# Performance work log

Measured on AMD Instinct MI355X. Metric: run time of the kernel, lower is better.

The kernel has to match this reference:

```python
import jax, jax.numpy as jnp
import numpy as np

H = 8          # attention heads
L = 2          # gnn_layers
D = 256        # embedding_size (= per-head out channels)
NEG_SLOPE = 0.2
LN_EPS = 1e-5


def setup_inputs() -> dict:
    key = jax.random.key(0)
    ks = jax.random.split(key, 10)
    B, N, E = 8, 4096, 131072
    node_embeddings = jax.random.normal(ks[0], (B, N, D), dtype=jnp.float32)
    edges = jax.random.randint(ks[1], (B, 2, E), 0, N, dtype=jnp.int64)
    s = 1.0 / np.sqrt(D)
    W       = jax.random.normal(ks[2], (L, H * D, D), dtype=jnp.float32) * s   # GATConv lin weight
    att_src = jax.random.normal(ks[3], (L, H, D), dtype=jnp.float32) * s
    att_dst = jax.random.normal(ks[4], (L, H, D), dtype=jnp.float32) * s
    gat_bias = jnp.zeros((L, H * D), dtype=jnp.float32)
    lin_W   = jax.random.normal(ks[5], (L, D, H * D), dtype=jnp.float32) * (1.0 / np.sqrt(H * D))
    lin_b   = jnp.zeros((L, D), dtype=jnp.float32)
    ln_gamma = jnp.ones((D,), dtype=jnp.float32)
    ln_beta  = jnp.zeros((D,), dtype=jnp.float32)
    return {"node_embeddings": node_embeddings, "edges": edges, "W": W,
            "att_src": att_src, "att_dst": att_dst, "gat_bias": gat_bias,
            "lin_W": lin_W, "lin_b": lin_b, "ln_gamma": ln_gamma, "ln_beta": ln_beta}


def _gat_conv(x, edge_index, Wl, a_src, a_dst, bias):
    # x: [N, D]; edge_index: [2, E] (row0 = src j, row1 = dst i)
    N = x.shape[0]
    loops = jnp.arange(N, dtype=edge_index.dtype)
    src = jnp.concatenate([edge_index[0], loops])   # PyG add_self_loops=True
    dst = jnp.concatenate([edge_index[1], loops])
    h = (x @ Wl.T).reshape(N, H, D)                 # [N, H, D]
    a_s = jnp.sum(h * a_src, axis=-1)               # [N, H]
    a_d = jnp.sum(h * a_dst, axis=-1)               # [N, H]
    e = jax.nn.leaky_relu(a_s[src] + a_d[dst], NEG_SLOPE)   # [E+N, H]
    # softmax over incoming edges of each destination node
    emax = jax.ops.segment_max(e, dst, num_segments=N)
    ex = jnp.exp(e - emax[dst])
    denom = jax.ops.segment_sum(ex, dst, num_segments=N)
    alpha = ex / (denom[dst] + 1e-16)               # [E+N, H]
    msg = h[src] * alpha[:, :, None]                # [E+N, H, D]
    out = jax.ops.segment_sum(msg, dst, num_segments=N)     # [N, H, D]
    return out.reshape(N, H * D) + bias


def _layer_norm(x, gamma, beta):
    mu = jnp.mean(x, axis=-1, keepdims=True)
    var = jnp.mean(jnp.square(x - mu), axis=-1, keepdims=True)
    return (x - mu) * jax.lax.rsqrt(var + LN_EPS) * gamma + beta


def reference(node_embeddings, edges, W, att_src, att_dst, gat_bias, lin_W, lin_b, ln_gamma, ln_beta):
    def per_graph(x, ei):
        h = x
        for l in range(L):
            res = h
            g = _gat_conv(h, ei, W[l], att_src[l], att_dst[l], gat_bias[l])
            g = g @ lin_W[l].T + lin_b[l]
            g = _layer_norm(g, ln_gamma, ln_beta)
            h = jax.nn.relu(g + res)   # dropout is identity at inference
        return h
    return jax.vmap(per_graph)(node_embeddings, edges)
```

## Files before the change

### kernel.cpp

```cpp
#include <hip/hip_runtime.h>
#include <hip/hip_bf16.h>

#define BB 8
#define NN 4096
#define EE 131072
#define ENL (EE + NN)
#define DD 256
#define HH 8
#define HD 2048
#define NPB (BB * NN)
#define CHUNK 16384
#define CAP 128

typedef __attribute__((ext_vector_type(8))) short bf16x8;
typedef __attribute__((ext_vector_type(4))) float f32x4;

static __device__ __forceinline__ float bf_lo(unsigned int u) { return __uint_as_float(u << 16); }
static __device__ __forceinline__ float bf_hi(unsigned int u) { return __uint_as_float(u & 0xFFFF0000u); }
static __device__ __forceinline__ unsigned short f2bf(float f) {
    __hip_bfloat16 h = __float2bfloat16(f);
    return *reinterpret_cast<unsigned short*>(&h);
}
static __device__ __forceinline__ unsigned int pack2(float a, float b) {
    return ((unsigned)f2bf(b) << 16) | f2bf(a);
}
static __device__ __forceinline__ void load_lds16(const void* g, void* l) {
    __builtin_amdgcn_global_load_lds(
        (const __attribute__((address_space(1))) unsigned int*)(g),
        (__attribute__((address_space(3))) unsigned int*)(l), 16, 0, 0);
}
static __device__ __forceinline__ float rl_f(float v, int lane) {
    return __uint_as_float(__builtin_amdgcn_readlane(__float_as_uint(v), lane));
}

__global__ void k_scatter(const int* __restrict__ edges, int* __restrict__ cnt, int* __restrict__ col) {
    int b = blockIdx.y;
    int idx = blockIdx.x * 256 + threadIdx.x;
    if (idx >= ENL) return;
    int src, dst;
    if (idx < EE) { src = edges[b*2*EE + idx]; dst = edges[b*2*EE + EE + idx]; }
    else { src = dst = idx - EE; }
    int g = b * NN + dst;
    int pos = atomicAdd(&cnt[g], 1);
    if (pos < CAP) col[(size_t)g * CAP + pos] = src;
}

__global__ __launch_bounds__(256) void k_prepA(const float* __restrict__ W, const float* __restrict__ linW,
                                               unsigned short* __restrict__ M2t,
                                               const float* __restrict__ asrc, const float* __restrict__ adst,
                                               float* __restrict__ wsatt, float* __restrict__ wdatt) {
    __shared__ float red[2][4][64];
    int bx = blockIdx.x;
    if (bx < 512) {
        int cb = bx & 31, h = (bx >> 5) & 7, l = bx >> 8;
        int d = threadIdx.x;
        const float* Bp = W + ((size_t)l * HD + h * DD) * DD;
        const float* Ap = linW + ((size_t)l * DD + cb * 8) * HD + h * DD;
        float acc[8] = {};
        for (int o = 0; o < DD; ++o) {
            float w = Bp[(size_t)o * DD + d];
            #pragma unroll
            for (int c = 0; c < 8; ++c)
                acc[c] = fmaf(Ap[(size_t)c * HD + o], w, acc[c]);
        }
        #pragma unroll
        for (int c = 0; c < 8; ++c)
            M2t[((size_t)l * DD + cb * 8 + c) * HD + h * DD + d] = f2bf(acc[c]);
    } else {
        int idx = bx - 512;
        int kb = idx & 3, h = (idx >> 2) & 7, l = idx >> 5;
        int k = threadIdx.x & 63, dg = threadIdx.x >> 6;
        float accs = 0.f, accd = 0.f;
        #pragma unroll 4
        for (int dd = 0; dd < 64; ++dd) {
            int d = dg * 64 + dd;
            float w = W[((size_t)l * HD + h * DD + d) * DD + kb * 64 + k];
            accs = fmaf(asrc[(l*HH + h)*DD + d], w, accs);
            accd = fmaf(adst[(l*HH + h)*DD + d], w, accd);
        }
        red[0][dg][k] = accs; red[1][dg][k] = accd;
        __syncthreads();
        int t = threadIdx.x;
        if (t < 64)
            wsatt[(l*HH + h)*DD + kb*64 + t] = red[0][0][t] + red[0][1][t] + red[0][2][t] + red[0][3][t];
        else if (t < 128) {
            int kk = t - 64;
            wdatt[(l*HH + h)*DD + kb*64 + kk] = red[1][0][kk] + red[1][1][kk] + red[1][2][kk] + red[1][3][kk];
        }
    }
}

__global__ __launch_bounds__(256) void k_prepB(const float* __restrict__ gbias, const float* __restrict__ linW,
                                               const float* __restrict__ linb, float* __restrict__ bias2,
                                               const float* __restrict__ ws, const float* __restrict__ wd,
                                               unsigned short* __restrict__ frag) {
    int bx = blockIdx.x;
    if (bx < 128) {
        int wv = threadIdx.x >> 6, lane = threadIdx.x & 63;
        int o = bx * 4 + wv;
        int l = o >> 8, c = o & 255;
        const float4* g4 = (const float4*)(gbias + l * HD);
        const float4* w4 = (const float4*)(linW + (size_t)l * DD * HD + (size_t)c * HD);
        float acc = 0.f;
        #pragma unroll
        for (int j = 0; j < 8; ++j) {
            float4 g = g4[j * 64 + lane]; float4 w = w4[j * 64 + lane];
            acc += g.x * w.x + g.y * w.y + g.z * w.z + g.w * w.w;
        }
        #pragma unroll
        for (int msk = 1; msk < 64; msk <<= 1) acc += __shfl_xor(acc, msk);
        if (lane == 0) bias2[o] = acc + linb[o];
    } else {
        int idx = bx - 128;
        int l = idx >> 1;
        int t = (idx & 1) * 256 + threadIdx.x;
        int ks = t >> 6, lane = t & 63, c = lane & 15, q = lane >> 4;
        #pragma unroll
        for (int j = 0; j < 8; ++j) {
            int k = ks * 32 + q * 8 + j;
            float v = (c < 8) ? ws[(l*HH + c)*DD + k] : wd[(l*HH + (c-8))*DD + k];
            frag[((size_t)l * 512 + t) * 8 + j] = f2bf(v);
        }
    }
}

__global__ void k_tobf(const float* __restrict__ X, uint2* __restrict__ xb2) {
    int idx = blockIdx.x * 256 + threadIdx.x;
    float4 v = *(const float4*)(X + (size_t)idx * 4);
    uint2 o; o.x = pack2(v.x, v.y); o.y = pack2(v.z, v.w);
    xb2[idx] = o;
}

__global__ __launch_bounds__(256) void k_attn_mfma(const unsigned short* __restrict__ xb,
                                                   const unsigned short* __restrict__ attfrag,
                                                   float* __restrict__ a_s, float* __restrict__ a_d) {
    int tid = threadIdx.x;
    int wv = tid >> 6, lane = tid & 63;
    int m0 = blockIdx.x * 64 + wv * 16;
    int c = lane & 15, q = lane >> 4;
    const unsigned short* arow = xb + (size_t)(m0 + c) * DD;
    f32x4 acc = (f32x4){0.f, 0.f, 0.f, 0.f};
    #pragma unroll
    for (int ks = 0; ks < 8; ++ks) {
        bf16x8 af = *(const bf16x8*)(arow + ks * 32 + q * 8);
        bf16x8 bf = *(const bf16x8*)(attfrag + (size_t)(ks * 64 + lane) * 8);
        acc = __builtin_amdgcn_mfma_f32_16x16x32_bf16(af, bf, acc, 0, 0, 0);
    }
    #pragma unroll
    for (int rg = 0; rg < 4; ++rg) {
        int row = m0 + q * 4 + rg;
        if (c < 8) a_s[row * 8 + c] = acc[rg];
        else       a_d[row * 8 + (c - 8)] = acc[rg];
    }
}

__global__ __launch_bounds__(256) void k_agg_y(const int* __restrict__ cnt, const int* __restrict__ col,
                                               const float* __restrict__ a_s, const float* __restrict__ a_d,
                                               const uint2* __restrict__ xb2, uint2* __restrict__ y2,
                                               int node0) {
    int wave = threadIdx.x >> 6, lane = threadIdx.x & 63;
    int blk = blockIdx.x;
    int xcd = blk & 7, q = blk >> 3;
    int gl = xcd >> 1;
    int sub = ((xcd & 1) << 9) | q;
    int g = node0 + gl * NN + sub * 4 + wave;
    int b = g >> 12;
    int re = cnt[g];
    const int* cl = col + (size_t)g * CAP;
    int gb = b * NN;
    int hl = lane & 7, slot = lane >> 3;
    float adh = a_d[(size_t)g * 8 + hl];
    float acc[8][4] = {};
    float sacc = 0.f;
    int nfull = re & ~7;
    for (int e0 = 0; e0 < nfull; e0 += 8) {
        int srcl = cl[e0 + slot];
        float sg = a_s[(size_t)(gb + srcl) * 8 + hl];
        int ss[8];
        #pragma unroll
        for (int i = 0; i < 8; ++i) ss[i] = __builtin_amdgcn_readlane(srcl, i * 8);
        uint2 u[8];
        #pragma unroll
        for (int i = 0; i < 8; ++i)
            u[i] = xb2[(size_t)(gb + ss[i]) * 64 + lane];
        float xs = sg + adh;
        xs = (xs > 0.f) ? xs : 0.2f * xs;
        float w = __expf(xs);
        sacc += w;
        #pragma unroll
        for (int i = 0; i < 8; ++i) {
            float x0 = bf_lo(u[i].x), x1 = bf_hi(u[i].x), x2 = bf_lo(u[i].y), x3 = bf_hi(u[i].y);
            #pragma unroll
            for (int h = 0; h < 8; ++h) {
                float wh = rl_f(w, i * 8 + h);
                acc[h][0] = fmaf(wh, x0, acc[h][0]);
                acc[h][1] = fmaf(wh, x1, acc[h][1]);
                acc[h][2] = fmaf(wh, x2, acc[h][2]);
                acc[h][3] = fmaf(wh, x3, acc[h][3]);
            }
        }
    }
    if (nfull < re) {
        int e = nfull + slot;
        bool valid = e < re;
        int srcl = valid ? cl[e] : 0;
        float w = 0.f;
        if (valid) {
            float xs = a_s[(size_t)(gb + srcl) * 8 + hl] + adh;
            xs = (xs > 0.f) ? xs : 0.2f * xs;
            w = __expf(xs);
        }
        sacc += w;
        int cntl = re - nfull;
        for (int i = 0; i < cntl; ++i) {
            int s = __builtin_amdgcn_readlane(srcl, i * 8);
            uint2 u = xb2[(size_t)(gb + s) * 64 + lane];
            float x0 = bf_lo(u.x), x1 = bf_hi(u.x), x2 = bf_lo(u.y), x3 = bf_hi(u.y);
            #pragma unroll
            for (int h = 0; h < 8; ++h) {
                float wh = rl_f(w, i * 8 + h);
                acc[h][0] = fmaf(wh, x0, acc[h][0]);
                acc[h][1] = fmaf(wh, x1, acc[h][1]);
                acc[h][2] = fmaf(wh, x2, acc[h][2]);
                acc[h][3] = fmaf(wh, x3, acc[h][3]);
            }
        }
    }
    sacc += __shfl_xor(sacc, 8);
    sacc += __shfl_xor(sacc, 16);
    sacc += __shfl_xor(sacc, 32);
    float rinv = 1.f / (sacc + 1e-16f);
    uint2* yr = y2 + (size_t)(g - node0) * 512 + lane;
    #pragma unroll
    for (int h = 0; h < 8; ++h) {
        float rh = rl_f(rinv, h);
        uint2 o;
        o.x = pack2(acc[h][0] * rh, acc[h][1] * rh);
        o.y = pack2(acc[h][2] * rh, acc[h][3] * rh);
        yr[h * 64] = o;
    }
}

__global__ __launch_bounds__(512) void k_gemm_ln(const unsigned short* __restrict__ Yb,
                                                 const unsigned short* __restrict__ Bt,
                                                 const float* __restrict__ bias2,
                                                 const float* __restrict__ gamma,
                                                 const float* __restrict__ beta,
                                                 const float* __restrict__ res,
                                                 float* __restrict__ out,
                                                 unsigned int* __restrict__ xb,
                                                 int node0) {
    __shared__ char lds[86528];
    int tid = threadIdx.x;
    int wv = tid >> 6, lane = tid & 63;
    int m0 = blockIdx.x * 64;
    int c = lane & 15, q = lane >> 4;
    f32x4 acc[4][2];
    #pragma unroll
    for (int mf = 0; mf < 4; ++mf)
        #pragma unroll
        for (int nf = 0; nf < 2; ++nf) acc[mf][nf] = (f32x4){0.f, 0.f, 0.f, 0.f};

    #define STAGE(BUF, KT) do {                                                        \
        int row_ = tid >> 3, j_ = tid & 7, jp_ = j_ ^ (row_ & 7);                      \
        load_lds16(Yb + (size_t)(m0 + row_) * HD + (KT) + jp_ * 8,                     \
                   lds + (BUF) * 40960 + wv * 1024);                                   \
        _Pragma("unroll")                                                              \
        for (int it_ = 0; it_ < 4; ++it_) {                                            \
            int ci_ = it_ * 512 + tid;                                                 \
            int br_ = ci_ >> 3, bj_ = ci_ & 7, bjp_ = bj_ ^ (br_ & 7);                 \
            load_lds16(Bt + (size_t)br_ * HD + (KT) + bjp_ * 8,                        \
                       lds + (BUF) * 40960 + 8192 + it_ * 8192 + wv * 1024);           \
        }                                                                              \
    } while (0)

    #define COMPUTE(BUF) do {                                                          \
        const char* Ab_ = lds + (BUF) * 40960;                                         \
        const char* Bb_ = lds + (BUF) * 40960 + 8192;                                  \
        _Pragma("unroll")                                                              \
        for (int ks = 0; ks < 2; ++ks) {                                               \
            int kb = ks * 64 + (q << 4);                                               \
            bf16x8 af[4], bfr[2];                                                      \
            _Pragma("unroll")                                                          \
            for (int mf = 0; mf < 4; ++mf) {                                           \
                int r = mf * 16 + c;                                                   \
                af[mf] = *(const bf16x8*)(Ab_ + r * 128 + (kb ^ ((r & 7) << 4)));      \
            }                                                                          \
            _Pragma("unroll")                                                          \
            for (int nf = 0; nf < 2; ++nf) {                                           \
                int nr = wv * 32 + nf * 16 + c;                                        \
                bfr[nf] = *(const bf16x8*)(Bb_ + nr * 128 + (kb ^ ((nr & 7) << 4)));   \
            }                                                                          \
            _Pragma("unroll")                                                          \
            for (int mf = 0; mf < 4; ++mf)                                             \
                _Pragma("unroll")                                                      \
                for (int nf = 0; nf < 2; ++nf)                                         \
                    acc[mf][nf] = __builtin_amdgcn_mfma_f32_16x16x32_bf16(             \
                        af[mf], bfr[nf], acc[mf][nf], 0, 0, 0);                        \
        }                                                                              \
    } while (0)

    STAGE(0, 0);
    __syncthreads();
    for (int t = 0; t < 32; t += 2) {
        if (t + 1 < 32) STAGE(1, (t + 1) * 64);
        COMPUTE(0);
        __syncthreads();
        if (t + 2 < 32) STAGE(0, (t + 2) * 64);
        COMPUTE(1);
        __syncthreads();
    }
    #undef STAGE
    #undef COMPUTE

    float2* lnbuf = (float2*)(lds + 81920);
    float2* musd  = (float2*)(lds + 86016);
    float b2[2], gmv[2], btv[2];
    #pragma unroll
    for (int nf = 0; nf < 2; ++nf) {
        int colx = wv * 32 + nf * 16 + c;
        b2[nf] = bias2[colx]; gmv[nf] = gamma[colx]; btv[nf] = beta[colx];
    }
    #pragma unroll
    for (int mf = 0; mf < 4; ++mf)
        #pragma unroll
        for (int nf = 0; nf < 2; ++nf)
            #pragma unroll
            for (int rg = 0; rg < 4; ++rg)
                acc[mf][nf][rg] += b2[nf];
    #pragma unroll
    for (int mf = 0; mf < 4; ++mf) {
        #pragma unroll
        for (int rg = 0; rg < 4; ++rg) {
            float s = 0.f, ss = 0.f;
            #pragma unroll
            for (int nf = 0; nf < 2; ++nf) { float v = acc[mf][nf][rg]; s += v; ss += v * v; }
            #pragma unroll
            for (int msk = 1; msk < 16; msk <<= 1) { s += __shfl_xor(s, msk); ss += __shfl_xor(ss, msk); }
            if (c == 0) lnbuf[(mf * 16 + q * 4 + rg) * 8 + wv] = make_float2(s, ss);
        }
    }
    __syncthreads();
    if (tid < 64) {
        float s = 0.f, ss = 0.f;
        #pragma unroll
        for (int w = 0; w < 8; ++w) { float2 p = lnbuf[tid * 8 + w]; s += p.x; ss += p.y; }
        float mu = s * (1.f / 256.f);
        float var = ss * (1.f / 256.f) - mu * mu;
        musd[tid] = make_float2(mu, rsqrtf(var + 1e-5f));
    }
    __syncthreads();
    #pragma unroll
    for (int mf = 0; mf < 4; ++mf) {
        #pragma unroll
        for (int rg = 0; rg < 4; ++rg) {
            int row = mf * 16 + q * 4 + rg;
            float2 ms = musd[row];
            size_t grow = (size_t)(node0 + m0 + row);
            #pragma unroll
            for (int nf = 0; nf < 2; ++nf) {
                int colx = wv * 32 + nf * 16 + c;
                float o = (acc[mf][nf][rg] - ms.x) * ms.y * gmv[nf] + btv[nf] + res[grow * DD + colx];
                o = fmaxf(o, 0.f);
                out[grow * DD + colx] = o;
                float nb = __shfl_xor(o, 1);
                if (!(c & 1)) xb[grow * 128 + (colx >> 1)] = pack2(o, nb);
            }
        }
    }
}

extern "C" void kernel_launch(void* const* d_in, const int* in_sizes, int n_in,
                              void* d_out, int out_size, void* d_ws, size_t ws_size,
                              hipStream_t stream) {
    const float* emb   = (const float*)d_in[0];
    const int*   edges = (const int*)d_in[1];
    const float* W     = (const float*)d_in[2];
    const float* asrc  = (const float*)d_in[3];
    const float* adst  = (const float*)d_in[4];
    const float* gbias = (const float*)d_in[5];
    const float* linW  = (const float*)d_in[6];
    const float* linb  = (const float*)d_in[7];
    const float* gam   = (const float*)d_in[8];
    const float* bet   = (const float*)d_in[9];
    float* out = (float*)d_out;

    char* ws = (char*)d_ws;
    uint2*          y2      = (uint2*)(ws + 0);
    uint2*          xb2     = (uint2*)(ws + 67108864);
    unsigned short* M2t     = (unsigned short*)(ws + 83886080);
    float*          wsatt   = (float*)(ws + 85983232);
    float*          wdatt   = (float*)(ws + 85999616);
    float*          bias2   = (float*)(ws + 86016000);
    float*          a_s     = (float*)(ws + 86018048);
    float*          a_d     = (float*)(ws + 87066624);
    int*            cnt     = (int*)(ws + 88115200);
    int*            colx    = (int*)(ws + 88246272);
    unsigned short* attfrag = (unsigned short*)(ws + 105023488);

    hipMemsetAsync(cnt, 0, NPB * sizeof(int), stream);
    k_scatter<<<dim3((ENL + 255) / 256, BB), 256, 0, stream>>>(edges, cnt, colx);
    k_prepA<<<dim3(576), 256, 0, stream>>>(W, linW, M2t, asrc, adst, wsatt, wdatt);
    k_prepB<<<dim3(132), 256, 0, stream>>>(gbias, linW, linb, bias2, wsatt, wdatt, attfrag);
    k_tobf<<<dim3(NPB * 64 / 256), 256, 0, stream>>>(emb, xb2);

    for (int l = 0; l < 2; ++l) {
        const float* X = (l == 0) ? emb : out;
        k_attn_mfma<<<dim3(NPB / 64), 256, 0, stream>>>((const unsigned short*)xb2,
                                                        attfrag + (size_t)l * 4096, a_s, a_d);
        for (int cc = 0; cc < 2; ++cc) {
            int node0 = cc * CHUNK;
            k_agg_y<<<dim3(CHUNK / 4), 256, 0, stream>>>(cnt, colx, a_s, a_d, xb2, y2, node0);
            k_gemm_ln<<<dim3(CHUNK / 64), 512, 0, stream>>>((const unsigned short*)y2,
                                                            M2t + (size_t)l * DD * HD, bias2 + l * DD,
                                                            gam, bet, X, out,
                                                            (unsigned int*)xb2, node0);
        }
    }
}
```

Baseline: 543.8 us.

## Rewrite edge aggregation as MFMA over 32-edge chunks staged in LDS

The per-node aggregation kernel now gathers source rows for 32 edges at a time straight into LDS using global_load_lds. It packs the 8 per-head attention weights into bf16 and computes the weighted sum with MFMA, reading the B operand through the transposing ds_read_b64_tr_b16. This replaces the scalar FMA loop and its many readlane broadcasts with matrix instructions. Because the attention weights are now rounded to bf16, and edge counts are padded to multiples of 32 with zero weights, it can waste work on low-degree nodes. The waits are fully serialized (vmcnt(0) and lgkmcnt(0) after each read), which limits overlap.

```diff
diff --git a/kernel.cpp b/kernel.cpp
--- a/kernel.cpp
+++ b/kernel.cpp
@@ -14,6 +14,7 @@
 
 typedef __attribute__((ext_vector_type(8))) short bf16x8;
 typedef __attribute__((ext_vector_type(4))) float f32x4;
+typedef __attribute__((ext_vector_type(2))) unsigned int u32x2;
 
 static __device__ __forceinline__ float bf_lo(unsigned int u) { return __uint_as_float(u << 16); }
 static __device__ __forceinline__ float bf_hi(unsigned int u) { return __uint_as_float(u & 0xFFFF0000u); }
@@ -28,9 +29,6 @@
     __builtin_amdgcn_global_load_lds(
         (const __attribute__((address_space(1))) unsigned int*)(g),
         (__attribute__((address_space(3))) unsigned int*)(l), 16, 0, 0);
-}
-static __device__ __forceinline__ float rl_f(float v, int lane) {
-    return __uint_as_float(__builtin_amdgcn_readlane(__float_as_uint(v), lane));
 }
 
 __global__ void k_scatter(const int* __restrict__ edges, int* __restrict__ cnt, int* __restrict__ col) {
@@ -154,90 +152,126 @@
     }
 }
 
-__global__ __launch_bounds__(256) void k_agg_y(const int* __restrict__ cnt, const int* __restrict__ col,
-                                               const float* __restrict__ a_s, const float* __restrict__ a_d,
-                                               const uint2* __restrict__ xb2, uint2* __restrict__ y2,
-                                               int node0) {
+__global__ __launch_bounds__(256) void k_agg_mfma(const int* __restrict__ cnt, const int* __restrict__ col,
+                                                  const float* __restrict__ a_s, const float* __restrict__ a_d,
+                                                  const uint2* __restrict__ xb2, uint2* __restrict__ y2,
+                                                  int node0) {
+    __shared__ char lds[33792];
     int wave = threadIdx.x >> 6, lane = threadIdx.x & 63;
+    char* wb = lds + wave * 8448;
+    unsigned wboff = (unsigned)(size_t)(__attribute__((address_space(3))) char*)wb;
+
     int blk = blockIdx.x;
     int xcd = blk & 7, q = blk >> 3;
     int gl = xcd >> 1;
     int sub = ((xcd & 1) << 9) | q;
     int g = node0 + gl * NN + sub * 4 + wave;
-    int b = g >> 12;
+    int b = g >> 12, gb = b * NN;
     int re = cnt[g];
     const int* cl = col + (size_t)g * CAP;
-    int gb = b * NN;
-    int hl = lane & 7, slot = lane >> 3;
-    float adh = a_d[(size_t)g * 8 + hl];
-    float acc[8][4] = {};
+
+    int sp = lane >> 3;
+    int e_sub = ((sp & 3) << 1) | (sp >> 2);
+    int e_lane = e_sub * 4 + ((lane & 7) >> 1);
+    int chalf = (lane & 1) * 16;
+    int hh = lane & 7;
+    float adh = a_d[(size_t)g * 8 + hh];
+    const char* xbase = (const char*)xb2;
+
+    unsigned vbase = wboff + lane * 8;
+
+    f32x4 acc[16];
+    #pragma unroll
+    for (int t = 0; t < 16; ++t) acc[t] = (f32x4){0.f, 0.f, 0.f, 0.f};
     float sacc = 0.f;
-    int nfull = re & ~7;
-    for (int e0 = 0; e0 < nfull; e0 += 8) {
-        int srcl = cl[e0 + slot];
-        float sg = a_s[(size_t)(gb + srcl) * 8 + hl];
-        int ss[8];
-        #pragma unroll
-        for (int i = 0; i < 8; ++i) ss[i] = __builtin_amdgcn_readlane(srcl, i * 8);
-        uint2 u[8];
+
+    for (int c0 = 0; c0 < re; c0 += 32) {
+        int se = c0 + e_lane; if (se > re - 1) se = re - 1;
+        int r = cl[se];
+        const char* src = xbase + ((size_t)(gb + r)) * 512 + chalf;
         #pragma unroll
         for (int i = 0; i < 8; ++i)
-            u[i] = xb2[(size_t)(gb + ss[i]) * 64 + lane];
-        float xs = sg + adh;
-        xs = (xs > 0.f) ? xs : 0.2f * xs;
-        float w = __expf(xs);
-        sacc += w;
-        #pragma unroll
-        for (int i = 0; i < 8; ++i) {
-            float x0 = bf_lo(u[i].x), x1 = bf_hi(u[i].x), x2 = bf_lo(u[i].y), x3 = bf_hi(u[i].y);
-            #pragma unroll
-            for (int h = 0; h < 8; ++h) {
-                float wh = rl_f(w, i * 8 + h);
-                acc[h][0] = fmaf(wh, x0, acc[h][0]);
-                acc[h][1] = fmaf(wh, x1, acc[h][1]);
-                acc[h][2] = fmaf(wh, x2, acc[h][2]);
-                acc[h][3] = fmaf(wh, x3, acc[h][3]);
-            }
-        }
-    }
-    if (nfull < re) {
-        int e = nfull + slot;
-        bool valid = e < re;
-        int srcl = valid ? cl[e] : 0;
-        float w = 0.f;
-        if (valid) {
-            float xs = a_s[(size_t)(gb + srcl) * 8 + hl] + adh;
+            load_lds16(src + i * 32, wb + i * 1024);
+
+        int kb = c0 + ((lane >> 4) << 3);
+        float w[8];
+        #pragma unroll
+        for (int j = 0; j < 8; ++j) {
+            int e = kb + j;
+            int ei = e; if (ei > re - 1) ei = re - 1;
+            int s = cl[ei];
+            float xs = a_s[(size_t)(gb + s) * 8 + hh] + adh;
             xs = (xs > 0.f) ? xs : 0.2f * xs;
-            w = __expf(xs);
-        }
-        sacc += w;
-        int cntl = re - nfull;
-        for (int i = 0; i < cntl; ++i) {
-            int s = __builtin_amdgcn_readlane(srcl, i * 8);
-            uint2 u = xb2[(size_t)(gb + s) * 64 + lane];
-            float x0 = bf_lo(u.x), x1 = bf_hi(u.x), x2 = bf_lo(u.y), x3 = bf_hi(u.y);
-            #pragma unroll
-            for (int h = 0; h < 8; ++h) {
-                float wh = rl_f(w, i * 8 + h);
-                acc[h][0] = fmaf(wh, x0, acc[h][0]);
-                acc[h][1] = fmaf(wh, x1, acc[h][1]);
-                acc[h][2] = fmaf(wh, x2, acc[h][2]);
-                acc[h][3] = fmaf(wh, x3, acc[h][3]);
-            }
-        }
-    }
-    sacc += __shfl_xor(sacc, 8);
+            float ww = (e < re) ? __expf(xs) : 0.f;
+            w[j] = ww;
+            sacc += ww;
+        }
+        union AU { unsigned u[4]; bf16x8 v; } au;
+        au.u[0] = pack2(w[0], w[1]); au.u[1] = pack2(w[2], w[3]);
+        au.u[2] = pack2(w[4], w[5]); au.u[3] = pack2(w[6], w[7]);
+        bf16x8 af = au.v;
+
+        asm volatile("s_waitcnt vmcnt(0)" ::: "memory");
+        __builtin_amdgcn_sched_barrier(0);
+        #pragma unroll
+        for (int t = 0; t < 8; ++t) {
+            u32x2 r1, r2;
+            unsigned vat = vbase + t * 1024;
+            asm volatile("ds_read_b64_tr_b16 %0, %2\n\t"
+                         "ds_read_b64_tr_b16 %1, %2 offset:512"
+                         : "=&v"(r1), "=&v"(r2) : "v"(vat));
+            asm volatile("s_waitcnt lgkmcnt(0)" ::: "memory");
+            __builtin_amdgcn_sched_barrier(0);
+            union BU { struct { u32x2 a, b; } p; bf16x8 v; } bu;
+            bu.p.a = r1; bu.p.b = r2;
+            acc[t] = __builtin_amdgcn_mfma_f32_16x16x32_bf16(af, bu.v, acc[t], 0, 0, 0);
+        }
+        #pragma unroll
+        for (int i = 0; i < 8; ++i)
+            load_lds16(src + (8 + i) * 32, wb + i * 1024);
+        asm volatile("s_waitcnt vmcnt(0)" ::: "memory");
+        __builtin_amdgcn_sched_barrier(0);
+        #pragma unroll
+        for (int t = 0; t < 8; ++t) {
+            u32x2 r1, r2;
+            unsigned vat = vbase + t * 1024;
+            asm volatile("ds_read_b64_tr_b16 %0, %2\n\t"
+                         "ds_read_b64_tr_b16 %1, %2 offset:512"
+                         : "=&v"(r1), "=&v"(r2) : "v"(vat));
+            asm volatile("s_waitcnt lgkmcnt(0)" ::: "memory");
+            __builtin_amdgcn_sched_barrier(0);
+            union BU { struct { u32x2 a, b; } p; bf16x8 v; } bu;
+            bu.p.a = r1; bu.p.b = r2;
+            acc[8 + t] = __builtin_amdgcn_mfma_f32_16x16x32_bf16(af, bu.v, acc[8 + t], 0, 0, 0);
+        }
+    }
+
     sacc += __shfl_xor(sacc, 16);
     sacc += __shfl_xor(sacc, 32);
     float rinv = 1.f / (sacc + 1e-16f);
-    uint2* yr = y2 + (size_t)(g - node0) * 512 + lane;
-    #pragma unroll
-    for (int h = 0; h < 8; ++h) {
-        float rh = rl_f(rinv, h);
-        uint2 o;
-        o.x = pack2(acc[h][0] * rh, acc[h][1] * rh);
-        o.y = pack2(acc[h][2] * rh, acc[h][3] * rh);
-        yr[h * 64] = o;
+    float rv[4];
+    #pragma unroll
+    for (int rg = 0; rg < 4; ++rg)
+        rv[rg] = __shfl(rinv, ((lane >> 4) & 1) * 4 + rg);
+
+    float* fb = (float*)wb;
+    if (lane < 32) {
+        int rbase = (lane >> 4) * 4;
+        #pragma unroll
+        for (int t = 0; t < 16; ++t) {
+            #pragma unroll
+            for (int rg = 0; rg < 4; ++rg)
+                fb[(rbase + rg) * 260 + t * 16 + (lane & 15)] = acc[t][rg] * rv[rg];
+        }
+    }
+    int h = lane >> 3, m = lane & 7;
+    const float* rowp = fb + h * 260;
+    char* yrow = (char*)y2 + ((size_t)(g - node0)) * 4096 + h * 512;
+    #pragma unroll
+    for (int k = 0; k < 8; ++k) {
+        float4 v = *(const float4*)(rowp + m * 4 + k * 32);
+        uint2 o; o.x = pack2(v.x, v.y); o.y = pack2(v.z, v.w);
+        *(uint2*)(yrow + m * 8 + k * 64) = o;
     }
 }
 
@@ -410,7 +444,7 @@
                                                         attfrag + (size_t)l * 4096, a_s, a_d);
         for (int cc = 0; cc < 2; ++cc) {
             int node0 = cc * CHUNK;
-            k_agg_y<<<dim3(CHUNK / 4), 256, 0, stream>>>(cnt, colx, a_s, a_d, xb2, y2, node0);
+            k_agg_mfma<<<dim3(CHUNK / 4), 256, 0, stream>>>(cnt, colx, a_s, a_d, xb2, y2, node0);
             k_gemm_ln<<<dim3(CHUNK / 64), 512, 0, stream>>>((const unsigned short*)y2,
                                                             M2t + (size_t)l * DD * HD, bias2 + l * DD,
                                                             gam, bet, X, out,
```

New measurement: 597.0 us. 9.8% more time.
